# Kernel tuning notes

Measured on AMD Instinct MI355X. Metric: run time of the kernel, lower is better.

## Reference

```python
import jax, jax.numpy as jnp
import numpy as np

EPS = 1e-5
N_NODES = 10
NUM_JOINTS = 6   # all robot_configs fixed to '3_segments_3DOF' (module's fallback default)
MAX_DOF = 10


def _lin(x, w, b):
    # torch nn.Linear: y = x @ W.T + b, W is (out, in)
    return jnp.einsum('...i,oi->...o', x, w) + b


def _layernorm(x, scale, bias):
    mu = x.mean(-1, keepdims=True)
    var = x.var(-1, keepdims=True)
    return (x - mu) / jnp.sqrt(var + EPS) * scale + bias


def _forward(images, text_lengths, node_features, edge_indices, p):
    B = images.shape[0]
    # --- SimplifiedVLMBackbone ---
    y = jax.lax.conv_general_dilated(images, p['conv_w'], (2, 2), [(3, 3), (3, 3)],
                                     dimension_numbers=('NCHW', 'OIHW', 'NCHW'))
    y = jax.nn.relu(y + p['conv_b'][None, :, None, None])          # (B,32,112,112)
    y = y.reshape(B, 32, 7, 16, 7, 16).mean(axis=(3, 5))            # adaptive avg pool -> (B,32,7,7)
    y = y.reshape(B, 32 * 49)
    y = jax.nn.relu(_lin(y, p['img_fc1_w'], p['img_fc1_b']))
    img_feat = _lin(y, p['img_fc2_w'], p['img_fc2_b'])               # (B,768)
    t = p['text_emb'][jnp.clip(text_lengths, 0, 9999)]               # (B,256)
    vlm = img_feat + _lin(t, p['text_fc_w'], p['text_fc_b'])         # (B,768)

    # --- SoftArmGraphNN ---
    x = jax.nn.relu(_lin(node_features, p['enc1_w'], p['enc1_b']))
    x = _lin(x, p['enc2_w'], p['enc2_b'])                            # (B,N,64)
    src, dst = edge_indices[:, 0, :], edge_indices[:, 1, :]          # (B,E)

    def agg_fn(xi, si, di):
        # mean of neighbor (source) features per destination node; 0 if no neighbors
        g = xi[si]                                                   # (E,D)
        s = jax.ops.segment_sum(g, di, num_segments=N_NODES)
        c = jax.ops.segment_sum(jnp.ones(di.shape, xi.dtype), di, num_segments=N_NODES)
        return s / jnp.maximum(c, 1.0)[:, None]

    for i in range(3):
        residual = x
        mean_nb = jax.vmap(agg_fn)(x, src, dst)                      # (B,N,64)
        comb = jnp.concatenate([x, mean_nb], axis=-1)                # (B,N,128)
        x = _lin(comb, p['gc_w'][i], p['gc_b'][i])
        x = jax.nn.relu(_layernorm(x + residual, p['ln_scale'][i], p['ln_bias'][i]))
    graph_tokens = _lin(x, p['proj_w'], p['proj_b'])                 # (B,N,32)

    # --- AttentionPooling + dual-path fusion ---
    s = _lin(jnp.tanh(_lin(graph_tokens, p['attn1_w'], p['attn1_b'])), p['attn2_w'], p['attn2_b'])
    w = jax.nn.softmax(s, axis=1)                                    # (B,N,1)
    robot_token = jnp.sum(graph_tokens * w, axis=1)                  # (B,32) -> project? 32 vs 768 -> residual add via broadcast pad
    fused = vlm.at[:, :robot_token.shape[-1]].add(robot_token)       # global token residual into vlm features

    # --- NodeActionHead (all samples: 3seg_3DOF -> 6 joints, per-joint MLPs) ---
    comb = jnp.concatenate([
        jnp.broadcast_to(fused[:, None, :], (B, NUM_JOINTS, fused.shape[-1])),
        graph_tokens[:, :NUM_JOINTS, :]], axis=-1)                   # (B,J,800)
    h = jax.nn.relu(jnp.einsum('bjf,jhf->bjh', comb, p['head_w1']) + p['head_b1'])
    h = jax.nn.relu(jnp.einsum('bjf,jhf->bjh', h, p['head_w2']) + p['head_b2'])
    a = jnp.einsum('bjf,jhf->bjh', h, p['head_w3']) + p['head_b3']   # (B,6,16)
    a = jnp.pad(a, ((0, 0), (0, MAX_DOF - NUM_JOINTS), (0, 0)))      # pad to max_dof
    return jnp.transpose(a, (0, 2, 1))                               # (B,16,10)


def setup_inputs() -> dict:
    key = jax.random.key(0)
    ks = iter(jax.random.split(key, 64))

    def nrm(shape, scale=0.02):
        return scale * jax.random.normal(next(ks), shape, dtype=jnp.float32)

    B = 128
    inp = {
        'images': jax.random.normal(next(ks), (B, 3, 224, 224), dtype=jnp.float32),
        'text_lengths': jax.random.randint(next(ks), (B,), 0, 10000, dtype=jnp.int32),
        'node_features': jax.random.normal(next(ks), (B, N_NODES, 19), dtype=jnp.float32),
        'edge_indices': jax.random.randint(next(ks), (B, 2, 18), 0, N_NODES, dtype=jnp.int32),
        'conv_w': nrm((32, 3, 7, 7)), 'conv_b': jnp.zeros(32, jnp.float32),
        'img_fc1_w': nrm((512, 1568)), 'img_fc1_b': jnp.zeros(512, jnp.float32),
        'img_fc2_w': nrm((768, 512)), 'img_fc2_b': jnp.zeros(768, jnp.float32),
        'text_emb': nrm((10000, 256)),
        'text_fc_w': nrm((768, 256)), 'text_fc_b': jnp.zeros(768, jnp.float32),
        'enc1_w': nrm((64, 19)), 'enc1_b': jnp.zeros(64, jnp.float32),
        'enc2_w': nrm((64, 64)), 'enc2_b': jnp.zeros(64, jnp.float32),
        'gc_w': nrm((3, 64, 128)), 'gc_b': jnp.zeros((3, 64), jnp.float32),
        'ln_scale': jnp.ones((3, 64), jnp.float32), 'ln_bias': jnp.zeros((3, 64), jnp.float32),
        'proj_w': nrm((32, 64)), 'proj_b': jnp.zeros(32, jnp.float32),
        'attn1_w': nrm((16, 32)), 'attn1_b': jnp.zeros(16, jnp.float32),
        'attn2_w': nrm((1, 16)), 'attn2_b': jnp.zeros(1, jnp.float32),
        'head_w1': nrm((6, 128, 800)), 'head_b1': jnp.zeros((6, 128), jnp.float32),
        'head_w2': nrm((6, 64, 128)), 'head_b2': jnp.zeros((6, 64), jnp.float32),
        'head_w3': nrm((6, 16, 64)), 'head_b3': jnp.zeros((6, 16), jnp.float32),
    }
    return inp


def reference(images, text_lengths, node_features, edge_indices, conv_w, conv_b,
              img_fc1_w, img_fc1_b, img_fc2_w, img_fc2_b, text_emb, text_fc_w, text_fc_b,
              enc1_w, enc1_b, enc2_w, enc2_b, gc_w, gc_b, ln_scale, ln_bias,
              proj_w, proj_b, attn1_w, attn1_b, attn2_w, attn2_b,
              head_w1, head_b1, head_w2, head_b2, head_w3, head_b3):
    p = dict(conv_w=conv_w, conv_b=conv_b, img_fc1_w=img_fc1_w, img_fc1_b=img_fc1_b,
             img_fc2_w=img_fc2_w, img_fc2_b=img_fc2_b, text_emb=text_emb,
             text_fc_w=text_fc_w, text_fc_b=text_fc_b, enc1_w=enc1_w, enc1_b=enc1_b,
             enc2_w=enc2_w, enc2_b=enc2_b, gc_w=gc_w, gc_b=gc_b, ln_scale=ln_scale,
             ln_bias=ln_bias, proj_w=proj_w, proj_b=proj_b, attn1_w=attn1_w,
             attn1_b=attn1_b, attn2_w=attn2_w, attn2_b=attn2_b, head_w1=head_w1,
             head_b1=head_b1, head_w2=head_w2, head_b2=head_b2, head_w3=head_w3,
             head_b3=head_b3)
    return _forward(images, text_lengths, node_features, edge_indices, p)
```

## Files before the change

### kernel.cpp

```cpp
#include <hip/hip_runtime.h>
#include <hip/hip_bf16.h>
#include <math.h>

typedef __attribute__((ext_vector_type(8))) short bf16x8;
typedef __attribute__((ext_vector_type(4))) float f32x4;

static __device__ __forceinline__ unsigned short f2bf(float f) {
    union { float f; unsigned int u; } x{f};
    unsigned int u = x.u;
    unsigned int r = (u + 0x7fffu + ((u >> 16) & 1u)) >> 16;
    return (unsigned short)r;
}

static __device__ __forceinline__ unsigned int pack2(float f0, float f1) {
    __hip_bfloat162 h = __float22bfloat162_rn(float2{f0, f1});
    union { __hip_bfloat162 h; unsigned int u; } c{h};
    return c.u;
}

__global__ __launch_bounds__(256) void wprep(const float* __restrict__ conv_w,
                                             unsigned short* __restrict__ wB) {
    for (int idx = threadIdx.x; idx < 24 * 32 * 8; idx += 256) {
        int s = idx >> 8;
        int ch = (idx >> 3) & 31;
        int kx = idx & 7;
        int c = s >> 3, ky = s & 7;
        float v = 0.f;
        if (ky < 7 && kx < 7) v = conv_w[ch * 147 + c * 49 + ky * 7 + kx];
        wB[idx] = f2bf(v);
    }
}

#define PSTRIDE 120
__global__ __launch_bounds__(512, 4) void conv_mfma(const float* __restrict__ img,
                                                    const unsigned int* __restrict__ wBu,
                                                    const float* __restrict__ cb,
                                                    float* __restrict__ pooledH) {
    __shared__ unsigned int patch[63 * PSTRIDE];
    const int t = threadIdx.x;
    const int py = blockIdx.x, half = blockIdx.y, b = blockIdx.z;
    const int B = gridDim.z;
    const int lane = t & 63, wid = t >> 6;
    const int r16 = lane & 15, g = lane >> 4;
    const int Y0 = 32 * py + 16 * half - 3;

    const int xc0 = 2 * lane - 3;
    const int xc1 = 2 * lane + 125;
    const int a00 = max(xc0, 0);
    const int a01 = max(xc0 + 1, 0);
    const int a10 = min(xc1, 223);
    const int a11 = min(xc1 + 1, 223);
    const bool v00 = (xc0 >= 0);
    const bool v01 = (xc0 + 1 >= 0);
    const bool v10 = (xc1 <= 223);
    const bool v11 = (xc1 + 1 <= 223);
    const bool c1act = (lane < 52);

    const float* ib = img + (size_t)b * 3 * 224 * 224;

#pragma unroll
    for (int hb = 0; hb < 2; ++hb) {
        float g0[4], g1[4], g2[4], g3[4];
        int rr[4];
        bool rv[4];
#pragma unroll
        for (int i = 0; i < 4; ++i) {
            int r = wid + 8 * (hb * 4 + i);
            int c_ = (r >= 42) ? 2 : ((r >= 21) ? 1 : 0);
            int pr = r - 21 * c_;
            int iy = Y0 + pr;
            rv[i] = (r < 63) & (iy >= 0) & (iy < 224);
            int iyc = min(max(iy, 0), 223);
            const float* rp = ib + (c_ * 224 + iyc) * 224;
            rr[i] = r;
            g0[i] = rp[a00];
            g1[i] = rp[a01];
            g2[i] = rp[a10];
            g3[i] = rp[a11];
        }
#pragma unroll
        for (int i = 0; i < 4; ++i) {
            float f0 = (rv[i] && v00) ? g0[i] : 0.f;
            float f1 = (rv[i] && v01) ? g1[i] : 0.f;
            float f2_ = (rv[i] && v10) ? g2[i] : 0.f;
            float f3 = (rv[i] && v11) ? g3[i] : 0.f;
            if (rr[i] < 63) {
                patch[rr[i] * PSTRIDE + lane] = pack2(f0, f1);
                if (c1act) patch[rr[i] * PSTRIDE + 64 + lane] = pack2(f2_, f3);
            }
        }
    }

    bf16x8 bfrA[6], bfrB[6];
    int rowoff[6];
#pragma unroll
    for (int k = 0; k < 6; ++k) {
        int s = 4 * k + g;
        int c = s >> 3, ky = s & 7;
        int kyc = ky > 6 ? 6 : ky;
        rowoff[k] = c * 21 + kyc;
        union { uint4 q; bf16x8 v; } ua, ub;
        ua.q = *(const uint4*)(wBu + (s * 32 + r16) * 4);
        ub.q = *(const uint4*)(wBu + (s * 32 + r16 + 16) * 4);
        bfrA[k] = ua.v;
        bfrB[k] = ub.v;
    }
    const float biasA = cb[r16], biasB = cb[r16 + 16];

    __syncthreads();

    float accA[7], accB[7];
    int rb[6];
#pragma unroll
    for (int k = 0; k < 6; ++k) rb[k] = (rowoff[k] + 2 * wid) * PSTRIDE;

    for (int t7 = 0; t7 < 7; ++t7) {
        const int oxr = 16 * t7 + r16;
        f32x4 C0 = {biasA, biasA, biasA, biasA};
        f32x4 C1 = {biasB, biasB, biasB, biasB};
#pragma unroll
        for (int k = 0; k < 6; ++k) {
            const unsigned int* ap = &patch[rb[k] + oxr];
            union { unsigned int u[4]; bf16x8 v; } ua;
            ua.u[0] = ap[0];
            ua.u[1] = ap[1];
            ua.u[2] = ap[2];
            ua.u[3] = ap[3];
            C0 = __builtin_amdgcn_mfma_f32_16x16x32_bf16(ua.v, bfrA[k], C0, 0, 0, 0);
            C1 = __builtin_amdgcn_mfma_f32_16x16x32_bf16(ua.v, bfrB[k], C1, 0, 0, 0);
        }
        float s0 = 0.f, s1 = 0.f;
#pragma unroll
        for (int r = 0; r < 4; ++r) {
            s0 += fmaxf(C0[r], 0.f);
            s1 += fmaxf(C1[r], 0.f);
        }
        accA[t7] = s0;
        accB[t7] = s1;
    }
#pragma unroll
    for (int p = 0; p < 7; ++p) {
        accA[p] += __shfl_xor(accA[p], 16);
        accA[p] += __shfl_xor(accA[p], 32);
        accB[p] += __shfl_xor(accB[p], 16);
        accB[p] += __shfl_xor(accB[p], 32);
    }
    __syncthreads();
    float* sw = (float*)patch;
    if (lane < 16) {
#pragma unroll
        for (int p = 0; p < 7; ++p) {
            sw[(wid * 7 + p) * 32 + lane] = accA[p];
            sw[(wid * 7 + p) * 32 + lane + 16] = accB[p];
        }
    }
    __syncthreads();
    if (t < 224) {
        int p = t >> 5, ch = t & 31;
        float s = 0.f;
#pragma unroll
        for (int w = 0; w < 8; ++w) s += sw[(w * 7 + p) * 32 + ch];
        pooledH[(size_t)(half * B + b) * 1568 + ch * 49 + py * 7 + p] = s * (1.f / 256.f);
    }
}

__global__ __launch_bounds__(256) void fc1_k(const float* __restrict__ in,
                                             const float* __restrict__ w,
                                             const float* __restrict__ bias,
                                             float* __restrict__ out, int B) {
    const int t = threadIdx.x, lane = t & 63, wid = t >> 6;
    const int qg = blockIdx.x & 31;
    const int bg = blockIdx.x >> 5;
    const int b0 = bg * 8;
    const int o0 = (qg * 4 + wid) * 4;
    const float4* wp = (const float4*)w;
    const float4* xp0 = (const float4*)in;
    const float4* xp1 = xp0 + (size_t)B * 392;

    float acc[4][8];
#pragma unroll
    for (int oo = 0; oo < 4; ++oo)
#pragma unroll
        for (int r = 0; r < 8; ++r) acc[oo][r] = 0.f;

    for (int i = lane; i < 392; i += 64) {
        float4 wv[4];
#pragma unroll
        for (int oo = 0; oo < 4; ++oo) wv[oo] = wp[(size_t)(o0 + oo) * 392 + i];
#pragma unroll
        for (int r = 0; r < 8; ++r) {
            float4 a = xp0[(size_t)(b0 + r) * 392 + i];
            float4 c = xp1[(size_t)(b0 + r) * 392 + i];
            float4 xv = {a.x + c.x, a.y + c.y, a.z + c.z, a.w + c.w};
#pragma unroll
            for (int oo = 0; oo < 4; ++oo) {
                acc[oo][r] = fmaf(xv.x, wv[oo].x, acc[oo][r]);
                acc[oo][r] = fmaf(xv.y, wv[oo].y, acc[oo][r]);
                acc[oo][r] = fmaf(xv.z, wv[oo].z, acc[oo][r]);
                acc[oo][r] = fmaf(xv.w, wv[oo].w, acc[oo][r]);
            }
        }
    }
#pragma unroll
    for (int oo = 0; oo < 4; ++oo) {
        float v = 0.f;
#pragma unroll
        for (int r = 0; r < 8; ++r) {
            float s = acc[oo][r];
            s += __shfl_xor(s, 32);
            s += __shfl_xor(s, 16);
            s += __shfl_xor(s, 8);
            s += __shfl_xor(s, 4);
            s += __shfl_xor(s, 2);
            s += __shfl_xor(s, 1);
            if (lane == r) v = s;
        }
        if (lane < 8)
            out[(size_t)(b0 + lane) * 512 + o0 + oo] = fmaxf(v + bias[o0 + oo], 0.f);
    }
}

__global__ __launch_bounds__(256) void vlm_k(const float* __restrict__ h1,
                                             const float* __restrict__ w2,
                                             const float* __restrict__ b2,
                                             const int* __restrict__ tlen,
                                             const float* __restrict__ temb,
                                             const float* __restrict__ tw,
                                             const float* __restrict__ tb,
                                             const float* __restrict__ rtok,
                                             float* __restrict__ fused) {
    const int t = threadIdx.x, lane = t & 63, wid = t >> 6;
    const int ogq = blockIdx.x % 48;
    const int bg = blockIdx.x / 48;
    const int b0 = bg * 8;
    const int o0 = (ogq * 4 + wid) * 4;

    int rows[8];
#pragma unroll
    for (int r = 0; r < 8; ++r) {
        int v = tlen[b0 + r];
        rows[r] = min(max(v, 0), 9999);
    }
    const float4* wp = (const float4*)w2;
    const float4* xp = (const float4*)h1;
    const float4* wtp = (const float4*)tw;
    const float4* xtp = (const float4*)temb;

    float acc[4][8];
#pragma unroll
    for (int oo = 0; oo < 4; ++oo)
#pragma unroll
        for (int r = 0; r < 8; ++r) acc[oo][r] = 0.f;

#pragma unroll
    for (int ii = 0; ii < 2; ++ii) {
        int i = lane + (ii << 6);
        float4 wv[4];
#pragma unroll
        for (int oo = 0; oo < 4; ++oo) wv[oo] = wp[(size_t)(o0 + oo) * 128 + i];
#pragma unroll
        for (int r = 0; r < 8; ++r) {
            float4 xv = xp[(size_t)(b0 + r) * 128 + i];
#pragma unroll
            for (int oo = 0; oo < 4; ++oo) {
                acc[oo][r] = fmaf(xv.x, wv[oo].x, acc[oo][r]);
                acc[oo][r] = fmaf(xv.y, wv[oo].y, acc[oo][r]);
                acc[oo][r] = fmaf(xv.z, wv[oo].z, acc[oo][r]);
                acc[oo][r] = fmaf(xv.w, wv[oo].w, acc[oo][r]);
            }
        }
    }
    {
        float4 wv[4];
#pragma unroll
        for (int oo = 0; oo < 4; ++oo) wv[oo] = wtp[(size_t)(o0 + oo) * 64 + lane];
#pragma unroll
        for (int r = 0; r < 8; ++r) {
            float4 xv = xtp[(size_t)rows[r] * 64 + lane];
#pragma unroll
            for (int oo = 0; oo < 4; ++oo) {
                acc[oo][r] = fmaf(xv.x, wv[oo].x, acc[oo][r]);
                acc[oo][r] = fmaf(xv.y, wv[oo].y, acc[oo][r]);
                acc[oo][r] = fmaf(xv.z, wv[oo].z, acc[oo][r]);
                acc[oo][r] = fmaf(xv.w, wv[oo].w, acc[oo][r]);
            }
        }
    }
#pragma unroll
    for (int oo = 0; oo < 4; ++oo) {
        float v = 0.f;
#pragma unroll
        for (int r = 0; r < 8; ++r) {
            float s = acc[oo][r];
            s += __shfl_xor(s, 32);
            s += __shfl_xor(s, 16);
            s += __shfl_xor(s, 8);
            s += __shfl_xor(s, 4);
            s += __shfl_xor(s, 2);
            s += __shfl_xor(s, 1);
            if (lane == r) v = s;
        }
        int o = o0 + oo;
        if (lane < 8) {
            float add = (o < 32) ? rtok[(size_t)(b0 + lane) * 32 + o] : 0.f;
            fused[(size_t)(b0 + lane) * 768 + o] = v + b2[o] + tb[o] + add;
        }
    }
}

__global__ __launch_bounds__(640, 1) void graph_k(
    const float* __restrict__ nfeat, const int* __restrict__ eidx,
    const float* __restrict__ e1w, const float* __restrict__ e1b,
    const float* __restrict__ e2w, const float* __restrict__ e2b,
    const float* __restrict__ gcw, const float* __restrict__ gcb,
    const float* __restrict__ lns, const float* __restrict__ lnb,
    const float* __restrict__ pjw, const float* __restrict__ pjb,
    const float* __restrict__ a1w, const float* __restrict__ a1b,
    const float* __restrict__ a2w, const float* __restrict__ a2b,
    float* __restrict__ gts_g, float* __restrict__ rtok) {
    __shared__ __align__(16) float pool[8448];
    __shared__ __align__(16) float nf[10][20];
    __shared__ __align__(16) float xsA[10][64];
    __shared__ __align__(16) float xsB[10][64];
    __shared__ __align__(16) float nbs[10][64];
    __shared__ __align__(16) float gtss[10][32];
    __shared__ float svs[10];
    __shared__ int se[18], de[18];
    const int t = threadIdx.x;
    const int b = blockIdx.x;
    const int n = t >> 6, o = t & 63;

    if (t < 190) {
        int nn = t / 19, i = t - nn * 19;
        nf[nn][i] = nfeat[(size_t)(b * 10 + nn) * 19 + i];
    }
    if (t < 36) {
        if (t < 18) se[t] = eidx[b * 36 + t];
        else de[t - 18] = eidx[b * 36 + t];
    }
    float* e1wT = pool;
    float* e2wT = pool + 1280;
    for (int u = t; u < 1216; u += 640) {
        int oo = u / 19, k = u - oo * 19;
        e1wT[k * 64 + oo] = e1w[u];
    }
    for (int u = t; u < 4096; u += 640) {
        int oo = u >> 6, k = u & 63;
        e2wT[k * 65 + oo] = e2w[u];
    }
    __syncthreads();

    {
        float acc = e1b[o];
#pragma unroll
        for (int i = 0; i < 19; ++i) acc = fmaf(nf[n][i], e1wT[i * 64 + o], acc);
        xsB[n][o] = fmaxf(acc, 0.f);
    }
    {
        const float* xrow = &xsB[n][0];
        float s0 = 0, s1 = 0, s2 = 0, s3 = 0;
#pragma unroll
        for (int k = 0; k < 64; k += 4) {
            s0 = fmaf(xrow[k], e2wT[k * 65 + o], s0);
            s1 = fmaf(xrow[k + 1], e2wT[(k + 1) * 65 + o], s1);
            s2 = fmaf(xrow[k + 2], e2wT[(k + 2) * 65 + o], s2);
            s3 = fmaf(xrow[k + 3], e2wT[(k + 3) * 65 + o], s3);
        }
        xsA[n][o] = e2b[o] + ((s0 + s1) + (s2 + s3));
    }
    __syncthreads();

    float* src = &xsA[0][0];
    float* dst = &xsB[0][0];
    for (int l = 0; l < 3; ++l) {
        const float* gl = gcw + (size_t)l * 8192;
        for (int u = t; u < 8192; u += 640) {
            int oo = u >> 7, k = u & 127;
            pool[k * 65 + oo] = gl[u];
        }
        {
            float s = 0.f;
            int cnt = 0;
#pragma unroll
            for (int e = 0; e < 18; ++e) {
                bool m = (de[e] == n);
                float v = src[se[e] * 64 + o];
                s += m ? v : 0.f;
                cnt += m ? 1 : 0;
            }
            nbs[n][o] = s / (float)(cnt > 1 ? cnt : 1);
        }
        __syncthreads();
        {
            const float* xa = src + n * 64;
            const float* xb = &nbs[n][0];
            float s0 = 0, s1 = 0, s2 = 0, s3 = 0;
#pragma unroll
            for (int k = 0; k < 64; k += 4) {
                s0 = fmaf(xa[k], pool[k * 65 + o], s0);
                s1 = fmaf(xa[k + 1], pool[(k + 1) * 65 + o], s1);
                s2 = fmaf(xa[k + 2], pool[(k + 2) * 65 + o], s2);
                s3 = fmaf(xa[k + 3], pool[(k + 3) * 65 + o], s3);
            }
#pragma unroll
            for (int k = 0; k < 64; k += 4) {
                s0 = fmaf(xb[k], pool[(64 + k) * 65 + o], s0);
                s1 = fmaf(xb[k + 1], pool[(64 + k + 1) * 65 + o], s1);
                s2 = fmaf(xb[k + 2], pool[(64 + k + 2) * 65 + o], s2);
                s3 = fmaf(xb[k + 3], pool[(64 + k + 3) * 65 + o], s3);
            }
            float v = gcb[l * 64 + o] + ((s0 + s1) + (s2 + s3)) + xa[o];
            float mu = v;
            mu += __shfl_xor(mu, 32);
            mu += __shfl_xor(mu, 16);
            mu += __shfl_xor(mu, 8);
            mu += __shfl_xor(mu, 4);
            mu += __shfl_xor(mu, 2);
            mu += __shfl_xor(mu, 1);
            mu *= (1.f / 64.f);
            float d = v - mu;
            float vr = d * d;
            vr += __shfl_xor(vr, 32);
            vr += __shfl_xor(vr, 16);
            vr += __shfl_xor(vr, 8);
            vr += __shfl_xor(vr, 4);
            vr += __shfl_xor(vr, 2);
            vr += __shfl_xor(vr, 1);
            vr *= (1.f / 64.f);
            dst[n * 64 + o] =
                fmaxf(d / sqrtf(vr + 1e-5f) * lns[l * 64 + o] + lnb[l * 64 + o], 0.f);
        }
        __syncthreads();
        float* tmp = src;
        src = dst;
        dst = tmp;
    }

    float* pjwT = pool;
    float* a1wT = pool + 2112;
    for (int u = t; u < 2048; u += 640) {
        int oo = u >> 6, k = u & 63;
        pjwT[k * 33 + oo] = pjw[u];
    }
    for (int u = t; u < 512; u += 640) {
        int hh = u >> 5, k = u & 31;
        a1wT[k * 17 + hh] = a1w[u];
    }
    __syncthreads();

    if (o < 32) {
        const float* xrow = src + n * 64;
        float s0 = 0, s1 = 0, s2 = 0, s3 = 0;
#pragma unroll
        for (int k = 0; k < 64; k += 4) {
            s0 = fmaf(xrow[k], pjwT[k * 33 + o], s0);
            s1 = fmaf(xrow[k + 1], pjwT[(k + 1) * 33 + o], s1);
            s2 = fmaf(xrow[k + 2], pjwT[(k + 2) * 33 + o], s2);
            s3 = fmaf(xrow[k + 3], pjwT[(k + 3) * 33 + o], s3);
        }
        float gv = pjb[o] + ((s0 + s1) + (s2 + s3));
        gtss[n][o] = gv;
        gts_g[(size_t)b * 320 + n * 32 + o] = gv;
    }
    if (o < 16) {
        const float* xrow = &gtss[n][0];
        float s0 = 0, s1 = 0, s2 = 0, s3 = 0;
#pragma unroll
        for (int k = 0; k < 32; k += 4) {
            s0 = fmaf(xrow[k], a1wT[k * 17 + o], s0);
            s1 = fmaf(xrow[k + 1], a1wT[(k + 1) * 17 + o], s1);
            s2 = fmaf(xrow[k + 2], a1wT[(k + 2) * 17 + o], s2);
            s3 = fmaf(xrow[k + 3], a1wT[(k + 3) * 17 + o], s3);
        }
        float z = a1b[o] + ((s0 + s1) + (s2 + s3));
        float sc = tanhf(z) * a2w[o];
        sc += __shfl_xor(sc, 8);
        sc += __shfl_xor(sc, 4);
        sc += __shfl_xor(sc, 2);
        sc += __shfl_xor(sc, 1);
        if (o == 0) svs[n] = sc + a2b[0];
    }
    __syncthreads();

    if (n == 0 && o < 32) {
        float m = svs[0];
#pragma unroll
        for (int i = 1; i < 10; ++i) m = fmaxf(m, svs[i]);
        float e[10];
        float sum = 0.f;
#pragma unroll
        for (int i = 0; i < 10; ++i) {
            e[i] = expf(svs[i] - m);
            sum += e[i];
        }
        float inv = 1.f / sum;
        float rt = 0.f;
#pragma unroll
        for (int nn = 0; nn < 10; ++nn) rt = fmaf(gtss[nn][o], e[nn] * inv, rt);
        rtok[(size_t)b * 32 + o] = rt;
    }
}

__global__ __launch_bounds__(256) void head1_k(const float* __restrict__ fused,
                                               const float* __restrict__ gts,
                                               const float* __restrict__ w1,
                                               const float* __restrict__ b1,
                                               float* __restrict__ h1T) {
    const int t = threadIdx.x, lane = t & 63, wid = t >> 6;
    const int ogq = blockIdx.x % 48;
    const int bg = blockIdx.x / 48;
    const int b0 = bg * 8;
    const int j = ogq >> 3;
    const int o0 = ogq * 16 + wid * 4;
    const float4* wp = (const float4*)w1;
    const float4* fp = (const float4*)fused;
    const float4* gp = (const float4*)gts;

    float acc[4][8];
#pragma unroll
    for (int oo = 0; oo < 4; ++oo)
#pragma unroll
        for (int r = 0; r < 8; ++r) acc[oo][r] = 0.f;

    for (int i = lane; i < 200; i += 64) {
        float4 wv[4];
#pragma unroll
        for (int oo = 0; oo < 4; ++oo) wv[oo] = wp[(size_t)(o0 + oo) * 200 + i];
#pragma unroll
        for (int r = 0; r < 8; ++r) {
            float4 xv = (i < 192) ? fp[(size_t)(b0 + r) * 192 + i]
                                  : gp[(size_t)(b0 + r) * 80 + j * 8 + (i - 192)];
#pragma unroll
            for (int oo = 0; oo < 4; ++oo) {
                acc[oo][r] = fmaf(xv.x, wv[oo].x, acc[oo][r]);
                acc[oo][r] = fmaf(xv.y, wv[oo].y, acc[oo][r]);
                acc[oo][r] = fmaf(xv.z, wv[oo].z, acc[oo][r]);
                acc[oo][r] = fmaf(xv.w, wv[oo].w, acc[oo][r]);
            }
        }
    }
#pragma unroll
    for (int oo = 0; oo < 4; ++oo) {
        float v = 0.f;
#pragma unroll
        for (int r = 0; r < 8; ++r) {
            float s = acc[oo][r];
            s += __shfl_xor(s, 32);
            s += __shfl_xor(s, 16);
            s += __shfl_xor(s, 8);
            s += __shfl_xor(s, 4);
            s += __shfl_xor(s, 2);
            s += __shfl_xor(s, 1);
            if (lane == r) v = s;
        }
        int o = o0 + oo;
        if (lane < 8) h1T[(size_t)o * 128 + b0 + lane] = fmaxf(v + b1[o], 0.f);
    }
}

__global__ __launch_bounds__(128) void head2_k(const float* __restrict__ h1T,
                                               const float* __restrict__ w2,
                                               const float* __restrict__ b2,
                                               float* __restrict__ h2T) {
    const int o2 = blockIdx.x;
    const int j = o2 >> 6;
    const int b = threadIdx.x;
    const float* wrow = w2 + (size_t)o2 * 128;
    const float* xcol = h1T + (size_t)j * 128 * 128 + b;
    float acc = b2[o2];
#pragma unroll 16
    for (int k = 0; k < 128; ++k) acc = fmaf(xcol[k * 128], wrow[k], acc);
    h2T[(size_t)o2 * 128 + b] = fmaxf(acc, 0.f);
}

__global__ __launch_bounds__(128) void head3_k(const float* __restrict__ h2T,
                                               const float* __restrict__ w3,
                                               const float* __restrict__ b3,
                                               float* __restrict__ out) {
    const int jj = blockIdx.x % 10;
    const int oo = blockIdx.x / 10;
    const int b = threadIdx.x;
    float acc = 0.f;
    if (jj < 6) {
        const float* wrow = w3 + (size_t)(jj * 16 + oo) * 64;
        const float* xcol = h2T + (size_t)jj * 64 * 128 + b;
        acc = b3[jj * 16 + oo];
#pragma unroll 16
        for (int k = 0; k < 64; ++k) acc = fmaf(xcol[k * 128], wrow[k], acc);
    }
    out[(size_t)b * 160 + oo * 10 + jj] = acc;
}

extern "C" void kernel_launch(void* const* d_in, const int* in_sizes, int n_in,
                              void* d_out, int out_size, void* d_ws, size_t ws_size,
                              hipStream_t stream) {
    const float* images = (const float*)d_in[0];
    const int* tlen = (const int*)d_in[1];
    const float* nfeat = (const float*)d_in[2];
    const int* eidx = (const int*)d_in[3];
    const float* conv_w = (const float*)d_in[4];
    const float* conv_b = (const float*)d_in[5];
    const float* fc1w = (const float*)d_in[6];
    const float* fc1b = (const float*)d_in[7];
    const float* fc2w = (const float*)d_in[8];
    const float* fc2b = (const float*)d_in[9];
    const float* temb = (const float*)d_in[10];
    const float* tfw = (const float*)d_in[11];
    const float* tfb = (const float*)d_in[12];
    const float* e1w = (const float*)d_in[13];
    const float* e1b = (const float*)d_in[14];
    const float* e2w = (const float*)d_in[15];
    const float* e2b = (const float*)d_in[16];
    const float* gcw = (const float*)d_in[17];
    const float* gcb = (const float*)d_in[18];
    const float* lns = (const float*)d_in[19];
    const float* lnb = (const float*)d_in[20];
    const float* pjw = (const float*)d_in[21];
    const float* pjb = (const float*)d_in[22];
    const float* a1w = (const float*)d_in[23];
    const float* a1b = (const float*)d_in[24];
    const float* a2w = (const float*)d_in[25];
    const float* a2b = (const float*)d_in[26];
    const float* w1 = (const float*)d_in[27];
    const float* b1 = (const float*)d_in[28];
    const float* w2 = (const float*)d_in[29];
    const float* b2 = (const float*)d_in[30];
    const float* w3 = (const float*)d_in[31];
    const float* b3 = (const float*)d_in[32];

    const int B = in_sizes[0] / (3 * 224 * 224);

    float* ws = (float*)d_ws;
    unsigned short* wB = (unsigned short*)d_ws;
    float* pooledH = ws + 3072;
    float* h1fc = pooledH + (size_t)2 * B * 1568;
    float* fused = h1fc + (size_t)B * 512;
    float* gts = fused + (size_t)B * 768;
    float* rtok = gts + (size_t)B * 320;
    float* h1T = pooledH;
    float* h2T = pooledH + 98304;

    wprep<<<1, 256, 0, stream>>>(conv_w, wB);
    conv_mfma<<<dim3(7, 2, B), 512, 0, stream>>>(images, (const unsigned int*)wB,
                                                 conv_b, pooledH);
    fc1_k<<<512, 256, 0, stream>>>(pooledH, fc1w, fc1b, h1fc, B);
    graph_k<<<B, 640, 0, stream>>>(nfeat, eidx, e1w, e1b, e2w, e2b, gcw, gcb,
                                   lns, lnb, pjw, pjb, a1w, a1b, a2w, a2b,
                                   gts, rtok);
    vlm_k<<<768, 256, 0, stream>>>(h1fc, fc2w, fc2b, tlen, temb, tfw, tfb,
                                   rtok, fused);
    head1_k<<<768, 256, 0, stream>>>(fused, gts, w1, b1, h1T);
    head2_k<<<384, 128, 0, stream>>>(h1T, w2, b2, h2T);
    head3_k<<<160, 128, 0, stream>>>(h2T, w3, b3, (float*)d_out);
}
```

Baseline: 128.0 us.

## Merge weight prep into graph kernel and duplicate conv patch for aligned LDS reads

The conv weight bf16 repacking now runs as an extra block of the graph kernel, which moves ahead of the conv, removing one kernel launch. The conv kernel keeps a second copy of the patch shifted by one element, so each lane can read its A fragment with two aligned 64-bit LDS loads instead of four 32-bit ones. This doubles the patch LDS footprint and the shared-memory stores. Occupancy may drop at 512 threads per block with four blocks requested.

```diff
diff --git a/kernel.cpp b/kernel.cpp
--- a/kernel.cpp
+++ b/kernel.cpp
@@ -18,297 +18,8 @@
     return c.u;
 }
 
-__global__ __launch_bounds__(256) void wprep(const float* __restrict__ conv_w,
-                                             unsigned short* __restrict__ wB) {
-    for (int idx = threadIdx.x; idx < 24 * 32 * 8; idx += 256) {
-        int s = idx >> 8;
-        int ch = (idx >> 3) & 31;
-        int kx = idx & 7;
-        int c = s >> 3, ky = s & 7;
-        float v = 0.f;
-        if (ky < 7 && kx < 7) v = conv_w[ch * 147 + c * 49 + ky * 7 + kx];
-        wB[idx] = f2bf(v);
-    }
-}
-
-#define PSTRIDE 120
-__global__ __launch_bounds__(512, 4) void conv_mfma(const float* __restrict__ img,
-                                                    const unsigned int* __restrict__ wBu,
-                                                    const float* __restrict__ cb,
-                                                    float* __restrict__ pooledH) {
-    __shared__ unsigned int patch[63 * PSTRIDE];
-    const int t = threadIdx.x;
-    const int py = blockIdx.x, half = blockIdx.y, b = blockIdx.z;
-    const int B = gridDim.z;
-    const int lane = t & 63, wid = t >> 6;
-    const int r16 = lane & 15, g = lane >> 4;
-    const int Y0 = 32 * py + 16 * half - 3;
-
-    const int xc0 = 2 * lane - 3;
-    const int xc1 = 2 * lane + 125;
-    const int a00 = max(xc0, 0);
-    const int a01 = max(xc0 + 1, 0);
-    const int a10 = min(xc1, 223);
-    const int a11 = min(xc1 + 1, 223);
-    const bool v00 = (xc0 >= 0);
-    const bool v01 = (xc0 + 1 >= 0);
-    const bool v10 = (xc1 <= 223);
-    const bool v11 = (xc1 + 1 <= 223);
-    const bool c1act = (lane < 52);
-
-    const float* ib = img + (size_t)b * 3 * 224 * 224;
-
-#pragma unroll
-    for (int hb = 0; hb < 2; ++hb) {
-        float g0[4], g1[4], g2[4], g3[4];
-        int rr[4];
-        bool rv[4];
-#pragma unroll
-        for (int i = 0; i < 4; ++i) {
-            int r = wid + 8 * (hb * 4 + i);
-            int c_ = (r >= 42) ? 2 : ((r >= 21) ? 1 : 0);
-            int pr = r - 21 * c_;
-            int iy = Y0 + pr;
-            rv[i] = (r < 63) & (iy >= 0) & (iy < 224);
-            int iyc = min(max(iy, 0), 223);
-            const float* rp = ib + (c_ * 224 + iyc) * 224;
-            rr[i] = r;
-            g0[i] = rp[a00];
-            g1[i] = rp[a01];
-            g2[i] = rp[a10];
-            g3[i] = rp[a11];
-        }
-#pragma unroll
-        for (int i = 0; i < 4; ++i) {
-            float f0 = (rv[i] && v00) ? g0[i] : 0.f;
-            float f1 = (rv[i] && v01) ? g1[i] : 0.f;
-            float f2_ = (rv[i] && v10) ? g2[i] : 0.f;
-            float f3 = (rv[i] && v11) ? g3[i] : 0.f;
-            if (rr[i] < 63) {
-                patch[rr[i] * PSTRIDE + lane] = pack2(f0, f1);
-                if (c1act) patch[rr[i] * PSTRIDE + 64 + lane] = pack2(f2_, f3);
-            }
-        }
-    }
-
-    bf16x8 bfrA[6], bfrB[6];
-    int rowoff[6];
-#pragma unroll
-    for (int k = 0; k < 6; ++k) {
-        int s = 4 * k + g;
-        int c = s >> 3, ky = s & 7;
-        int kyc = ky > 6 ? 6 : ky;
-        rowoff[k] = c * 21 + kyc;
-        union { uint4 q; bf16x8 v; } ua, ub;
-        ua.q = *(const uint4*)(wBu + (s * 32 + r16) * 4);
-        ub.q = *(const uint4*)(wBu + (s * 32 + r16 + 16) * 4);
-        bfrA[k] = ua.v;
-        bfrB[k] = ub.v;
-    }
-    const float biasA = cb[r16], biasB = cb[r16 + 16];
-
-    __syncthreads();
-
-    float accA[7], accB[7];
-    int rb[6];
-#pragma unroll
-    for (int k = 0; k < 6; ++k) rb[k] = (rowoff[k] + 2 * wid) * PSTRIDE;
-
-    for (int t7 = 0; t7 < 7; ++t7) {
-        const int oxr = 16 * t7 + r16;
-        f32x4 C0 = {biasA, biasA, biasA, biasA};
-        f32x4 C1 = {biasB, biasB, biasB, biasB};
-#pragma unroll
-        for (int k = 0; k < 6; ++k) {
-            const unsigned int* ap = &patch[rb[k] + oxr];
-            union { unsigned int u[4]; bf16x8 v; } ua;
-            ua.u[0] = ap[0];
-            ua.u[1] = ap[1];
-            ua.u[2] = ap[2];
-            ua.u[3] = ap[3];
-            C0 = __builtin_amdgcn_mfma_f32_16x16x32_bf16(ua.v, bfrA[k], C0, 0, 0, 0);
-            C1 = __builtin_amdgcn_mfma_f32_16x16x32_bf16(ua.v, bfrB[k], C1, 0, 0, 0);
-        }
-        float s0 = 0.f, s1 = 0.f;
-#pragma unroll
-        for (int r = 0; r < 4; ++r) {
-            s0 += fmaxf(C0[r], 0.f);
-            s1 += fmaxf(C1[r], 0.f);
-        }
-        accA[t7] = s0;
-        accB[t7] = s1;
-    }
-#pragma unroll
-    for (int p = 0; p < 7; ++p) {
-        accA[p] += __shfl_xor(accA[p], 16);
-        accA[p] += __shfl_xor(accA[p], 32);
-        accB[p] += __shfl_xor(accB[p], 16);
-        accB[p] += __shfl_xor(accB[p], 32);
-    }
-    __syncthreads();
-    float* sw = (float*)patch;
-    if (lane < 16) {
-#pragma unroll
-        for (int p = 0; p < 7; ++p) {
-            sw[(wid * 7 + p) * 32 + lane] = accA[p];
-            sw[(wid * 7 + p) * 32 + lane + 16] = accB[p];
-        }
-    }
-    __syncthreads();
-    if (t < 224) {
-        int p = t >> 5, ch = t & 31;
-        float s = 0.f;
-#pragma unroll
-        for (int w = 0; w < 8; ++w) s += sw[(w * 7 + p) * 32 + ch];
-        pooledH[(size_t)(half * B + b) * 1568 + ch * 49 + py * 7 + p] = s * (1.f / 256.f);
-    }
-}
-
-__global__ __launch_bounds__(256) void fc1_k(const float* __restrict__ in,
-                                             const float* __restrict__ w,
-                                             const float* __restrict__ bias,
-                                             float* __restrict__ out, int B) {
-    const int t = threadIdx.x, lane = t & 63, wid = t >> 6;
-    const int qg = blockIdx.x & 31;
-    const int bg = blockIdx.x >> 5;
-    const int b0 = bg * 8;
-    const int o0 = (qg * 4 + wid) * 4;
-    const float4* wp = (const float4*)w;
-    const float4* xp0 = (const float4*)in;
-    const float4* xp1 = xp0 + (size_t)B * 392;
-
-    float acc[4][8];
-#pragma unroll
-    for (int oo = 0; oo < 4; ++oo)
-#pragma unroll
-        for (int r = 0; r < 8; ++r) acc[oo][r] = 0.f;
-
-    for (int i = lane; i < 392; i += 64) {
-        float4 wv[4];
-#pragma unroll
-        for (int oo = 0; oo < 4; ++oo) wv[oo] = wp[(size_t)(o0 + oo) * 392 + i];
-#pragma unroll
-        for (int r = 0; r < 8; ++r) {
-            float4 a = xp0[(size_t)(b0 + r) * 392 + i];
-            float4 c = xp1[(size_t)(b0 + r) * 392 + i];
-            float4 xv = {a.x + c.x, a.y + c.y, a.z + c.z, a.w + c.w};
-#pragma unroll
-            for (int oo = 0; oo < 4; ++oo) {
-                acc[oo][r] = fmaf(xv.x, wv[oo].x, acc[oo][r]);
-                acc[oo][r] = fmaf(xv.y, wv[oo].y, acc[oo][r]);
-                acc[oo][r] = fmaf(xv.z, wv[oo].z, acc[oo][r]);
-                acc[oo][r] = fmaf(xv.w, wv[oo].w, acc[oo][r]);
-            }
-        }
-    }
-#pragma unroll
-    for (int oo = 0; oo < 4; ++oo) {
-        float v = 0.f;
-#pragma unroll
-        for (int r = 0; r < 8; ++r) {
-            float s = acc[oo][r];
-            s += __shfl_xor(s, 32);
-            s += __shfl_xor(s, 16);
-            s += __shfl_xor(s, 8);
-            s += __shfl_xor(s, 4);
-            s += __shfl_xor(s, 2);
-            s += __shfl_xor(s, 1);
-            if (lane == r) v = s;
-        }
-        if (lane < 8)
-            out[(size_t)(b0 + lane) * 512 + o0 + oo] = fmaxf(v + bias[o0 + oo], 0.f);
-    }
-}
-
-__global__ __launch_bounds__(256) void vlm_k(const float* __restrict__ h1,
-                                             const float* __restrict__ w2,
-                                             const float* __restrict__ b2,
-                                             const int* __restrict__ tlen,
-                                             const float* __restrict__ temb,
-                                             const float* __restrict__ tw,
-                                             const float* __restrict__ tb,
-                                             const float* __restrict__ rtok,
-                                             float* __restrict__ fused) {
-    const int t = threadIdx.x, lane = t & 63, wid = t >> 6;
-    const int ogq = blockIdx.x % 48;
-    const int bg = blockIdx.x / 48;
-    const int b0 = bg * 8;
-    const int o0 = (ogq * 4 + wid) * 4;
-
-    int rows[8];
-#pragma unroll
-    for (int r = 0; r < 8; ++r) {
-        int v = tlen[b0 + r];
-        rows[r] = min(max(v, 0), 9999);
-    }
-    const float4* wp = (const float4*)w2;
-    const float4* xp = (const float4*)h1;
-    const float4* wtp = (const float4*)tw;
-    const float4* xtp = (const float4*)temb;
-
-    float acc[4][8];
-#pragma unroll
-    for (int oo = 0; oo < 4; ++oo)
-#pragma unroll
-        for (int r = 0; r < 8; ++r) acc[oo][r] = 0.f;
-
-#pragma unroll
-    for (int ii = 0; ii < 2; ++ii) {
-        int i = lane + (ii << 6);
-        float4 wv[4];
-#pragma unroll
-        for (int oo = 0; oo < 4; ++oo) wv[oo] = wp[(size_t)(o0 + oo) * 128 + i];
-#pragma unroll
-        for (int r = 0; r < 8; ++r) {
-            float4 xv = xp[(size_t)(b0 + r) * 128 + i];
-#pragma unroll
-            for (int oo = 0; oo < 4; ++oo) {
-                acc[oo][r] = fmaf(xv.x, wv[oo].x, acc[oo][r]);
-                acc[oo][r] = fmaf(xv.y, wv[oo].y, acc[oo][r]);
-                acc[oo][r] = fmaf(xv.z, wv[oo].z, acc[oo][r]);
-                acc[oo][r] = fmaf(xv.w, wv[oo].w, acc[oo][r]);
-            }
-        }
-    }
-    {
-        float4 wv[4];
-#pragma unroll
-        for (int oo = 0; oo < 4; ++oo) wv[oo] = wtp[(size_t)(o0 + oo) * 64 + lane];
-#pragma unroll
-        for (int r = 0; r < 8; ++r) {
-            float4 xv = xtp[(size_t)rows[r] * 64 + lane];
-#pragma unroll
-            for (int oo = 0; oo < 4; ++oo) {
-                acc[oo][r] = fmaf(xv.x, wv[oo].x, acc[oo][r]);
-                acc[oo][r] = fmaf(xv.y, wv[oo].y, acc[oo][r]);
-                acc[oo][r] = fmaf(xv.z, wv[oo].z, acc[oo][r]);
-                acc[oo][r] = fmaf(xv.w, wv[oo].w, acc[oo][r]);
-            }
-        }
-    }
-#pragma unroll
-    for (int oo = 0; oo < 4; ++oo) {
-        float v = 0.f;
-#pragma unroll
-        for (int r = 0; r < 8; ++r) {
-            float s = acc[oo][r];
-            s += __shfl_xor(s, 32);
-            s += __shfl_xor(s, 16);
-            s += __shfl_xor(s, 8);
-            s += __shfl_xor(s, 4);
-            s += __shfl_xor(s, 2);
-            s += __shfl_xor(s, 1);
-            if (lane == r) v = s;
-        }
-        int o = o0 + oo;
-        if (lane < 8) {
-            float add = (o < 32) ? rtok[(size_t)(b0 + lane) * 32 + o] : 0.f;
-            fused[(size_t)(b0 + lane) * 768 + o] = v + b2[o] + tb[o] + add;
-        }
-    }
-}
-
-__global__ __launch_bounds__(640, 1) void graph_k(
+__global__ __launch_bounds__(640, 1) void graph_wprep(
+    const float* __restrict__ conv_w, unsigned short* __restrict__ wB,
     const float* __restrict__ nfeat, const int* __restrict__ eidx,
     const float* __restrict__ e1w, const float* __restrict__ e1b,
     const float* __restrict__ e2w, const float* __restrict__ e2b,
@@ -317,7 +28,7 @@
     const float* __restrict__ pjw, const float* __restrict__ pjb,
     const float* __restrict__ a1w, const float* __restrict__ a1b,
     const float* __restrict__ a2w, const float* __restrict__ a2b,
-    float* __restrict__ gts_g, float* __restrict__ rtok) {
+    float* __restrict__ gts_g, float* __restrict__ rtok, int B) {
     __shared__ __align__(16) float pool[8448];
     __shared__ __align__(16) float nf[10][20];
     __shared__ __align__(16) float xsA[10][64];
@@ -329,6 +40,19 @@
     const int t = threadIdx.x;
     const int b = blockIdx.x;
     const int n = t >> 6, o = t & 63;
+
+    if (b == B) {
+        for (int idx = t; idx < 24 * 32 * 8; idx += 640) {
+            int s = idx >> 8;
+            int ch = (idx >> 3) & 31;
+            int kx = idx & 7;
+            int c = s >> 3, ky = s & 7;
+            float v = 0.f;
+            if (ky < 7 && kx < 7) v = conv_w[ch * 147 + c * 49 + ky * 7 + kx];
+            wB[idx] = f2bf(v);
+        }
+        return;
+    }
 
     if (t < 190) {
         int nn = t / 19, i = t - nn * 19;
@@ -498,6 +222,294 @@
 #pragma unroll
         for (int nn = 0; nn < 10; ++nn) rt = fmaf(gtss[nn][o], e[nn] * inv, rt);
         rtok[(size_t)b * 32 + o] = rt;
+    }
+}
+
+#define PSTRIDE 120
+#define PHALF (63 * PSTRIDE)
+__global__ __launch_bounds__(512, 4) void conv_mfma(const float* __restrict__ img,
+                                                    const unsigned int* __restrict__ wBu,
+                                                    const float* __restrict__ cb,
+                                                    float* __restrict__ pooledH) {
+    __shared__ __align__(16) unsigned int patch[2 * PHALF];
+    const int t = threadIdx.x;
+    const int py = blockIdx.x, half = blockIdx.y, b = blockIdx.z;
+    const int B = gridDim.z;
+    const int lane = t & 63, wid = t >> 6;
+    const int r16 = lane & 15, g = lane >> 4;
+    const int Y0 = 32 * py + 16 * half - 3;
+
+    const int xc0 = 2 * lane - 3;
+    const int xc1 = 2 * lane + 125;
+    const int a00 = max(xc0, 0);
+    const int a01 = max(xc0 + 1, 0);
+    const int a10 = min(xc1, 223);
+    const int a11 = min(xc1 + 1, 223);
+    const bool v00 = (xc0 >= 0);
+    const bool v01 = (xc0 + 1 >= 0);
+    const bool v10 = (xc1 <= 223);
+    const bool v11 = (xc1 + 1 <= 223);
+    const bool c1act = (lane < 52);
+
+    const float* ib = img + (size_t)b * 3 * 224 * 224;
+
+#pragma unroll
+    for (int hb = 0; hb < 2; ++hb) {
+        float g0[4], g1[4], g2[4], g3[4];
+        int rr[4];
+        bool rv[4];
+#pragma unroll
+        for (int i = 0; i < 4; ++i) {
+            int r = wid + 8 * (hb * 4 + i);
+            int c_ = (r >= 42) ? 2 : ((r >= 21) ? 1 : 0);
+            int pr = r - 21 * c_;
+            int iy = Y0 + pr;
+            rv[i] = (r < 63) & (iy >= 0) & (iy < 224);
+            int iyc = min(max(iy, 0), 223);
+            const float* rp = ib + (c_ * 224 + iyc) * 224;
+            rr[i] = r;
+            g0[i] = rp[a00];
+            g1[i] = rp[a01];
+            g2[i] = rp[a10];
+            g3[i] = rp[a11];
+        }
+#pragma unroll
+        for (int i = 0; i < 4; ++i) {
+            float f0 = (rv[i] && v00) ? g0[i] : 0.f;
+            float f1 = (rv[i] && v01) ? g1[i] : 0.f;
+            float f2_ = (rv[i] && v10) ? g2[i] : 0.f;
+            float f3 = (rv[i] && v11) ? g3[i] : 0.f;
+            if (rr[i] < 63) {
+                unsigned int v01p = pack2(f0, f1);
+                unsigned int v23p = pack2(f2_, f3);
+                patch[rr[i] * PSTRIDE + lane] = v01p;
+                if (lane >= 1) patch[PHALF + rr[i] * PSTRIDE + lane - 1] = v01p;
+                if (c1act) {
+                    patch[rr[i] * PSTRIDE + 64 + lane] = v23p;
+                    patch[PHALF + rr[i] * PSTRIDE + 63 + lane] = v23p;
+                }
+            }
+        }
+    }
+
+    bf16x8 bfrA[6], bfrB[6];
+    int rowoff[6];
+#pragma unroll
+    for (int k = 0; k < 6; ++k) {
+        int s = 4 * k + g;
+        int c = s >> 3, ky = s & 7;
+        int kyc = ky > 6 ? 6 : ky;
+        rowoff[k] = c * 21 + kyc;
+        union { uint4 q; bf16x8 v; } ua, ub;
+        ua.q = *(const uint4*)(wBu + (s * 32 + r16) * 4);
+        ub.q = *(const uint4*)(wBu + (s * 32 + r16 + 16) * 4);
+        bfrA[k] = ua.v;
+        bfrB[k] = ub.v;
+    }
+    const float biasA = cb[r16], biasB = cb[r16 + 16];
+
+    __syncthreads();
+
+    const int sel = r16 & 1;
+    const unsigned int* pbase = patch + sel * PHALF;
+    float accA[7], accB[7];
+    int rb[6];
+#pragma unroll
+    for (int k = 0; k < 6; ++k) rb[k] = (rowoff[k] + 2 * wid) * PSTRIDE;
+
+    for (int t7 = 0; t7 < 7; ++t7) {
+        const int idx0 = 16 * t7 + r16 - sel;
+        f32x4 C0 = {biasA, biasA, biasA, biasA};
+        f32x4 C1 = {biasB, biasB, biasB, biasB};
+#pragma unroll
+        for (int k = 0; k < 6; ++k) {
+            const uint2* ap2 = (const uint2*)(pbase + rb[k] + idx0);
+            uint2 q0 = ap2[0];
+            uint2 q1 = ap2[1];
+            union { unsigned int u[4]; bf16x8 v; } ua;
+            ua.u[0] = q0.x;
+            ua.u[1] = q0.y;
+            ua.u[2] = q1.x;
+            ua.u[3] = q1.y;
+            C0 = __builtin_amdgcn_mfma_f32_16x16x32_bf16(ua.v, bfrA[k], C0, 0, 0, 0);
+            C1 = __builtin_amdgcn_mfma_f32_16x16x32_bf16(ua.v, bfrB[k], C1, 0, 0, 0);
+        }
+        float s0 = 0.f, s1 = 0.f;
+#pragma unroll
+        for (int r = 0; r < 4; ++r) {
+            s0 += fmaxf(C0[r], 0.f);
+            s1 += fmaxf(C1[r], 0.f);
+        }
+        accA[t7] = s0;
+        accB[t7] = s1;
+    }
+#pragma unroll
+    for (int p = 0; p < 7; ++p) {
+        accA[p] += __shfl_xor(accA[p], 16);
+        accA[p] += __shfl_xor(accA[p], 32);
+        accB[p] += __shfl_xor(accB[p], 16);
+        accB[p] += __shfl_xor(accB[p], 32);
+    }
+    __syncthreads();
+    float* sw = (float*)patch;
+    if (lane < 16) {
+#pragma unroll
+        for (int p = 0; p < 7; ++p) {
+            sw[(wid * 7 + p) * 32 + lane] = accA[p];
+            sw[(wid * 7 + p) * 32 + lane + 16] = accB[p];
+        }
+    }
+    __syncthreads();
+    if (t < 224) {
+        int p = t >> 5, ch = t & 31;
+        float s = 0.f;
+#pragma unroll
+        for (int w = 0; w < 8; ++w) s += sw[(w * 7 + p) * 32 + ch];
+        pooledH[(size_t)(half * B + b) * 1568 + ch * 49 + py * 7 + p] = s * (1.f / 256.f);
+    }
+}
+
+__global__ __launch_bounds__(256) void fc1_k(const float* __restrict__ in,
+                                             const float* __restrict__ w,
+                                             const float* __restrict__ bias,
+                                             float* __restrict__ out, int B) {
+    const int t = threadIdx.x, lane = t & 63, wid = t >> 6;
+    const int qg = blockIdx.x & 31;
+    const int bg = blockIdx.x >> 5;
+    const int b0 = bg * 8;
+    const int o0 = (qg * 4 + wid) * 4;
+    const float4* wp = (const float4*)w;
+    const float4* xp0 = (const float4*)in;
+    const float4* xp1 = xp0 + (size_t)B * 392;
+
+    float acc[4][8];
+#pragma unroll
+    for (int oo = 0; oo < 4; ++oo)
+#pragma unroll
+        for (int r = 0; r < 8; ++r) acc[oo][r] = 0.f;
+
+    for (int i = lane; i < 392; i += 64) {
+        float4 wv[4];
+#pragma unroll
+        for (int oo = 0; oo < 4; ++oo) wv[oo] = wp[(size_t)(o0 + oo) * 392 + i];
+#pragma unroll
+        for (int r = 0; r < 8; ++r) {
+            float4 a = xp0[(size_t)(b0 + r) * 392 + i];
+            float4 c = xp1[(size_t)(b0 + r) * 392 + i];
+            float4 xv = {a.x + c.x, a.y + c.y, a.z + c.z, a.w + c.w};
+#pragma unroll
+            for (int oo = 0; oo < 4; ++oo) {
+                acc[oo][r] = fmaf(xv.x, wv[oo].x, acc[oo][r]);
+                acc[oo][r] = fmaf(xv.y, wv[oo].y, acc[oo][r]);
+                acc[oo][r] = fmaf(xv.z, wv[oo].z, acc[oo][r]);
+                acc[oo][r] = fmaf(xv.w, wv[oo].w, acc[oo][r]);
+            }
+        }
+    }
+#pragma unroll
+    for (int oo = 0; oo < 4; ++oo) {
+        float v = 0.f;
+#pragma unroll
+        for (int r = 0; r < 8; ++r) {
+            float s = acc[oo][r];
+            s += __shfl_xor(s, 32);
+            s += __shfl_xor(s, 16);
+            s += __shfl_xor(s, 8);
+            s += __shfl_xor(s, 4);
+            s += __shfl_xor(s, 2);
+            s += __shfl_xor(s, 1);
+            if (lane == r) v = s;
+        }
+        if (lane < 8)
+            out[(size_t)(b0 + lane) * 512 + o0 + oo] = fmaxf(v + bias[o0 + oo], 0.f);
+    }
+}
+
+__global__ __launch_bounds__(256) void vlm_k(const float* __restrict__ h1,
+                                             const float* __restrict__ w2,
+                                             const float* __restrict__ b2,
+                                             const int* __restrict__ tlen,
+                                             const float* __restrict__ temb,
+                                             const float* __restrict__ tw,
+                                             const float* __restrict__ tb,
+                                             const float* __restrict__ rtok,
+                                             float* __restrict__ fused) {
+    const int t = threadIdx.x, lane = t & 63, wid = t >> 6;
+    const int ogq = blockIdx.x % 48;
+    const int bg = blockIdx.x / 48;
+    const int b0 = bg * 8;
+    const int o0 = (ogq * 4 + wid) * 4;
+
+    int rows[8];
+#pragma unroll
+    for (int r = 0; r < 8; ++r) {
+        int v = tlen[b0 + r];
+        rows[r] = min(max(v, 0), 9999);
+    }
+    const float4* wp = (const float4*)w2;
+    const float4* xp = (const float4*)h1;
+    const float4* wtp = (const float4*)tw;
+    const float4* xtp = (const float4*)temb;
+
+    float acc[4][8];
+#pragma unroll
+    for (int oo = 0; oo < 4; ++oo)
+#pragma unroll
+        for (int r = 0; r < 8; ++r) acc[oo][r] = 0.f;
+
+#pragma unroll
+    for (int ii = 0; ii < 2; ++ii) {
+        int i = lane + (ii << 6);
+        float4 wv[4];
+#pragma unroll
+        for (int oo = 0; oo < 4; ++oo) wv[oo] = wp[(size_t)(o0 + oo) * 128 + i];
+#pragma unroll
+        for (int r = 0; r < 8; ++r) {
+            float4 xv = xp[(size_t)(b0 + r) * 128 + i];
+#pragma unroll
+            for (int oo = 0; oo < 4; ++oo) {
+                acc[oo][r] = fmaf(xv.x, wv[oo].x, acc[oo][r]);
+                acc[oo][r] = fmaf(xv.y, wv[oo].y, acc[oo][r]);
+                acc[oo][r] = fmaf(xv.z, wv[oo].z, acc[oo][r]);
+                acc[oo][r] = fmaf(xv.w, wv[oo].w, acc[oo][r]);
+            }
+        }
+    }
+    {
+        float4 wv[4];
+#pragma unroll
+        for (int oo = 0; oo < 4; ++oo) wv[oo] = wtp[(size_t)(o0 + oo) * 64 + lane];
+#pragma unroll
+        for (int r = 0; r < 8; ++r) {
+            float4 xv = xtp[(size_t)rows[r] * 64 + lane];
+#pragma unroll
+            for (int oo = 0; oo < 4; ++oo) {
+                acc[oo][r] = fmaf(xv.x, wv[oo].x, acc[oo][r]);
+                acc[oo][r] = fmaf(xv.y, wv[oo].y, acc[oo][r]);
+                acc[oo][r] = fmaf(xv.z, wv[oo].z, acc[oo][r]);
+                acc[oo][r] = fmaf(xv.w, wv[oo].w, acc[oo][r]);
+            }
+        }
+    }
+#pragma unroll
+    for (int oo = 0; oo < 4; ++oo) {
+        float v = 0.f;
+#pragma unroll
+        for (int r = 0; r < 8; ++r) {
+            float s = acc[oo][r];
+            s += __shfl_xor(s, 32);
+            s += __shfl_xor(s, 16);
+            s += __shfl_xor(s, 8);
+            s += __shfl_xor(s, 4);
+            s += __shfl_xor(s, 2);
+            s += __shfl_xor(s, 1);
+            if (lane == r) v = s;
+        }
+        int o = o0 + oo;
+        if (lane < 8) {
+            float add = (o < 32) ? rtok[(size_t)(b0 + lane) * 32 + o] : 0.f;
+            fused[(size_t)(b0 + lane) * 768 + o] = v + b2[o] + tb[o] + add;
+        }
     }
 }
 
@@ -640,13 +652,13 @@
     float* h1T = pooledH;
     float* h2T = pooledH + 98304;
 
-    wprep<<<1, 256, 0, stream>>>(conv_w, wB);
+    graph_wprep<<<B + 1, 640, 0, stream>>>(conv_w, wB, nfeat, eidx,
+                                           e1w, e1b, e2w, e2b, gcw, gcb,
+                                           lns, lnb, pjw, pjb, a1w, a1b,
+                                           a2w, a2b, gts, rtok, B);
     conv_mfma<<<dim3(7, 2, B), 512, 0, stream>>>(images, (const unsigned int*)wB,
                                                  conv_b, pooledH);
     fc1_k<<<512, 256, 0, stream>>>(pooledH, fc1w, fc1b, h1fc, B);
-    graph_k<<<B, 640, 0, stream>>>(nfeat, eidx, e1w, e1b, e2w, e2b, gcw, gcb,
-                                   lns, lnb, pjw, pjb, a1w, a1b, a2w, a2b,
-                                   gts, rtok);
     vlm_k<<<768, 256, 0, stream>>>(h1fc, fc2w, fc2b, tlen, temb, tfw, tfb,
                                    rtok, fused);
     head1_k<<<768, 256, 0, stream>>>(fused, gts, w1, b1, h1T);
```

New measurement: 119.7 us, median of 2. 1.07x faster.
